# Optimization experiments

Measured on AMD Instinct MI355X. Metric: run time of the kernel, lower is better.

The kernel has to match this reference:

```python
import jax, jax.numpy as jnp
import numpy as np

N_NODES = 50000
N_REL = 3
N_EDGES = 800000
D_FEAT = 128
D_HID = 128  # == dim_embs so residual + concat dims line up
D_QUERY = 64


def setup_inputs() -> dict:
    key = jax.random.key(0)
    ks = jax.random.split(key, 8)
    s = 1.0 / np.sqrt(D_HID)
    return {
        "x": jax.random.normal(ks[0], (N_NODES, D_FEAT), dtype=jnp.float32),
        "edges": jax.random.randint(ks[1], (N_REL, 2, N_EDGES), 0, N_NODES, dtype=jnp.int64),
        "feat_w": jax.random.normal(ks[2], (D_FEAT, D_HID), dtype=jnp.float32) * s,
        "conv_w": jax.random.normal(ks[3], (2, N_REL, D_HID, D_HID), dtype=jnp.float32) * s,
        "conv_b": jax.random.normal(ks[4], (2, N_REL, D_HID), dtype=jnp.float32) * 0.01,
        "attn_w": jax.random.normal(ks[5], (2, D_HID, D_QUERY), dtype=jnp.float32) * s,
        "attn_q": jax.random.normal(ks[6], (2, D_QUERY), dtype=jnp.float32) * s,
        "concat_w": jax.random.normal(ks[7], (D_HID, 3 * D_HID), dtype=jnp.float32) * s,
    }


def reference(x, edges, feat_w, conv_w, conv_b, attn_w, attn_q, concat_w):
    N = x.shape[0]
    R = edges.shape[0]
    ones_e = jnp.ones((edges.shape[2],), dtype=x.dtype)

    def gconv(h, src, dst, W, b):
        # GraphConv with symmetric ('both') normalization + residual
        deg_out = jnp.clip(jax.ops.segment_sum(ones_e, src, num_segments=N), 1.0)
        deg_in = jnp.clip(jax.ops.segment_sum(ones_e, dst, num_segments=N), 1.0)
        m = (h * jax.lax.rsqrt(deg_out)[:, None]) @ W          # [N, D]
        agg = jax.ops.segment_sum(m[src], dst, num_segments=N)  # gather-scatter [E, D] -> [N, D]
        return agg * jax.lax.rsqrt(deg_in)[:, None] + b + h

    def het_layer(h, l):
        # per-relation conv, then attention-weighted aggregation across relations
        vals = jnp.stack([gconv(h, edges[r, 0], edges[r, 1], conv_w[l, r], conv_b[l, r])
                          for r in range(R)])                   # [R, N, D]
        keys = jnp.tanh(jnp.einsum('rnd,dq->rnq', vals, attn_w[l]))
        scores = jnp.einsum('rnq,q->rn', keys, attn_q[l])       # [R, N]
        attn = jax.nn.softmax(scores, axis=0)                   # softmax over relations
        return jnp.einsum('rn,rnd->nd', attn, vals), attn

    h0 = jnp.tanh(x @ feat_w)            # feature_trans + tanh
    h1, _ = het_layer(h0, 1)             # 1-hop path (convs[1] only)
    t, _ = het_layer(h0, 0)              # 2-hop path: convs[0]
    h2, attn = het_layer(t, 1)           # then convs[1]
    y = jnp.concatenate([h0, h1, h2], axis=-1) @ concat_w.T  # concat_weight (no bias)
    return y, attn.T                      # attn_res: [N, R]
```

## Files before the change

### kernel.cpp

```cpp
#include <hip/hip_runtime.h>

#define NN 50000
#define NE 800000
#define DD 128
#define DQ 64
#define NB 42
#define SL 19048
#define NW 25000

typedef __attribute__((ext_vector_type(8))) short short8_t;
typedef __attribute__((ext_vector_type(4))) float f32x4;

__device__ __forceinline__ int clampi(int v, int lo, int hi) {
  return v < lo ? lo : (v > hi ? hi : v);
}
__device__ __forceinline__ unsigned short f2bf(float f) {
  unsigned int u = __float_as_uint(f);
  return (unsigned short)((u + 0x7FFFu + ((u >> 16) & 1u)) >> 16);
}
__device__ __forceinline__ float bfl(unsigned int u) { return __uint_as_float(u << 16); }
__device__ __forceinline__ float bfh(unsigned int u) { return __uint_as_float(u & 0xFFFF0000u); }
__device__ __forceinline__ float b2f(short s) {
  return __uint_as_float(((unsigned int)(unsigned short)s) << 16);
}

__global__ __launch_bounds__(512) void hist6_kernel(
    const int* __restrict__ e, unsigned int* __restrict__ hist,
    unsigned short* __restrict__ rank) {
  __shared__ unsigned int lds[NW];
  const int b = blockIdx.x;
  const int c = blockIdx.y;
  const int r = c >> 1;
  const int a = c & 1;
  const int tid = threadIdx.x;
  for (int i = tid; i < NW; i += 512) lds[i] = 0u;
  __syncthreads();
  const size_t abase = (size_t)r * 2 * NE + (a ? 0 : NE);
  const int beg = b * SL, end = min(beg + SL, NE);
  if (a == 0) {
    unsigned short* rk = rank + (size_t)r * NE;
    for (int i = beg + tid; i < end; i += 512) {
      int v = clampi(e[abase + i], 0, NN - 1);
      unsigned int sh = (v & 1) * 16;
      unsigned int old = atomicAdd(&lds[v >> 1], 1u << sh);
      rk[i] = (unsigned short)((old >> sh) & 0xFFFFu);
    }
  } else {
    for (int i = beg + tid; i < end; i += 512) {
      int v = clampi(e[abase + i], 0, NN - 1);
      atomicAdd(&lds[v >> 1], 1u << ((v & 1) * 16));
    }
  }
  __syncthreads();
  unsigned int* outp = hist + ((size_t)c * NB + b) * NW;
  for (int i = tid; i < NW; i += 512) outp[i] = lds[i];
}

__global__ __launch_bounds__(256) void sumscan_kernel(
    const unsigned int* __restrict__ hist, int* __restrict__ rowptr,
    int* __restrict__ btot, float* __restrict__ rsqi, float* __restrict__ rsqo) {
  __shared__ int part[256];
  const int g = blockIdx.x;
  const int c = blockIdx.y;
  const int r = c >> 1, a = c & 1;
  const int t = threadIdx.x;
  int cntv[8];
  int s = 0;
  const int w0 = g * 1000 + t * 4;
  if (t < 250) {
#pragma unroll
    for (int j = 0; j < 4; ++j) {
      const unsigned int* hp = hist + (size_t)c * NB * NW + w0 + j;
      unsigned int lo = 0, hi = 0;
#pragma unroll 7
      for (int b = 0; b < NB; ++b) {
        unsigned int v = hp[(size_t)b * NW];
        lo += v & 0xFFFFu;
        hi += v >> 16;
      }
      cntv[2 * j] = (int)lo;
      cntv[2 * j + 1] = (int)hi;
      int n0 = 2 * (w0 + j), n1 = n0 + 1;
      float f0 = rsqrtf(fmaxf((float)lo, 1.0f));
      float f1 = rsqrtf(fmaxf((float)hi, 1.0f));
      if (a == 0) {
        rsqi[r * NN + n0] = f0;
        rsqi[r * NN + n1] = f1;
      } else {
        rsqo[r * NN + n0] = f0;
        rsqo[r * NN + n1] = f1;
      }
      s += (int)(lo + hi);
    }
  }
  if (a == 1) return;
  part[t] = s;
  __syncthreads();
  for (int off = 1; off < 256; off <<= 1) {
    int x = (t >= off) ? part[t - off] : 0;
    __syncthreads();
    part[t] += x;
    __syncthreads();
  }
  if (t < 250) {
    int excl = part[t] - s;
    int base = g * 2000 + t * 8;
#pragma unroll
    for (int j = 0; j < 8; ++j) {
      rowptr[r * (NN + 1) + base + j] = excl;
      excl += cntv[j];
    }
  }
  if (t == 255) btot[r * 25 + g] = part[255];
}

__global__ __launch_bounds__(64) void scanp2_kernel(
    const int* __restrict__ btot, int* __restrict__ boff, int* __restrict__ rowptr) {
  if (threadIdx.x == 0) {
    for (int r = 0; r < 3; ++r) {
      int run = 0;
      for (int b = 0; b < 25; ++b) {
        boff[r * 25 + b] = run;
        run += btot[r * 25 + b];
      }
      rowptr[r * (NN + 1) + NN] = run;
    }
  }
}

__global__ __launch_bounds__(256) void bases_kernel(
    const unsigned int* __restrict__ hist, const int* __restrict__ boff,
    int* __restrict__ rowptr, int* __restrict__ bases) {
  const int r = blockIdx.y;
  const int off = boff[r * 25 + blockIdx.x];
  for (int wl = threadIdx.x; wl < 1000; wl += 256) {
    int w = blockIdx.x * 1000 + wl;
    int n0 = 2 * w, n1 = n0 + 1;
    int run0 = rowptr[r * (NN + 1) + n0] + off;
    int run1 = rowptr[r * (NN + 1) + n1] + off;
    rowptr[r * (NN + 1) + n0] = run0;
    rowptr[r * (NN + 1) + n1] = run1;
    const unsigned int* hp = hist + (size_t)(r * 2) * NB * NW + w;
    int* bp = bases + (size_t)r * NB * NN;
#pragma unroll 7
    for (int b = 0; b < NB; ++b) {
      unsigned int v = hp[(size_t)b * NW];
      bp[(size_t)b * NN + n0] = run0;
      bp[(size_t)b * NN + n1] = run1;
      run0 += (int)(v & 0xFFFFu);
      run1 += (int)(v >> 16);
    }
  }
}

__global__ __launch_bounds__(256) void fillr_kernel(
    const int* __restrict__ e, const unsigned short* __restrict__ rank,
    const int* __restrict__ bases, int* __restrict__ col) {
  const int r = blockIdx.y;
  const int i = blockIdx.x * 256 + threadIdx.x;
  const size_t sbase = (size_t)r * 2 * NE;
  int s = clampi(e[sbase + i], 0, NN - 1);
  int d = clampi(e[sbase + NE + i], 0, NN - 1);
  int b = i / SL;
  int pos = clampi(bases[((size_t)r * NB + b) * NN + d] + (int)rank[(size_t)r * NE + i],
                   0, NE - 1);
  col[(size_t)r * NE + pos] = s;
}

__global__ __launch_bounds__(256) void prepw_kernel(
    const float* __restrict__ conv_w, const float* __restrict__ feat_w,
    const float* __restrict__ concat_w, const float* __restrict__ attn_w,
    unsigned short* __restrict__ fw) {
  const int i = blockIdx.x;
  if (i < 10) {
    unsigned short* dst = fw + (size_t)i * 16384;
    for (int e = threadIdx.x; e < 2048; e += 256) {
      int nt = e >> 8, ks = (e >> 6) & 3, lane = e & 63;
      int n = (lane & 15) + nt * 16;
      int kb = (lane >> 4) * 8 + ks * 32;
      unsigned int w[4];
#pragma unroll
      for (int jj = 0; jj < 4; ++jj) {
        int k0 = kb + 2 * jj, k1 = k0 + 1;
        float f0, f1;
        if (i < 6) {
          f0 = conv_w[(size_t)i * 16384 + (size_t)k0 * DD + n];
          f1 = conv_w[(size_t)i * 16384 + (size_t)k1 * DD + n];
        } else if (i == 6) {
          f0 = feat_w[(size_t)k0 * DD + n];
          f1 = feat_w[(size_t)k1 * DD + n];
        } else {
          int p = i - 7;
          f0 = concat_w[(size_t)n * 384 + p * DD + k0];
          f1 = concat_w[(size_t)n * 384 + p * DD + k1];
        }
        w[jj] = (unsigned int)f2bf(f0) | ((unsigned int)f2bf(f1) << 16);
      }
      ((uint4*)dst)[e] = make_uint4(w[0], w[1], w[2], w[3]);
    }
  } else {
    const int l = i - 10;
    unsigned short* dst = fw + (size_t)10 * 16384 + (size_t)l * 8192;
    for (int e = threadIdx.x; e < 1024; e += 256) {
      int nt = e >> 8, ks = (e >> 6) & 3, lane = e & 63;
      int n = (lane & 15) + nt * 16;
      int kb = (lane >> 4) * 8 + ks * 32;
      unsigned int w[4];
#pragma unroll
      for (int jj = 0; jj < 4; ++jj) {
        int k0 = kb + 2 * jj, k1 = k0 + 1;
        float f0 = attn_w[((size_t)l * DD + k0) * DQ + n];
        float f1 = attn_w[((size_t)l * DD + k1) * DQ + n];
        w[jj] = (unsigned int)f2bf(f0) | ((unsigned int)f2bf(f1) << 16);
      }
      ((uint4*)dst)[e] = make_uint4(w[0], w[1], w[2], w[3]);
    }
  }
}

template <int AFP32, int TANH, int EPI, int SIX>
__global__ __launch_bounds__(256) void mgemm_kernel(
    const void* __restrict__ Ap, const unsigned short* __restrict__ fw,
    const float* __restrict__ rsqi, const float* __restrict__ bias,
    const unsigned short* __restrict__ residb, unsigned short* __restrict__ Cb) {
  const size_t ND = (size_t)NN * DD;
  const int rel = blockIdx.y;
  const int wsel = SIX ? (rel + 3) % 6 : rel;
  const int arel = SIX ? rel % 3 : rel;
  const unsigned short* fwp = fw + (size_t)wsel * 16384;
  const float* rsqip = EPI ? rsqi + (size_t)arel * NN : nullptr;
  const float* biasp = EPI ? bias + (size_t)wsel * DD : nullptr;
  unsigned short* Cbp = Cb + (size_t)rel * ND;
  __shared__ unsigned short sF[16384];
  const int tid = threadIdx.x;
  {
    const float4* s = (const float4*)fwp;
    float4* d = (float4*)sF;
#pragma unroll
    for (int i = 0; i < 8; ++i) d[tid + i * 256] = s[tid + i * 256];
  }
  __syncthreads();
  const int w = tid >> 6, l = tid & 63, la = l & 15, gr = l >> 4;
  const int row0 = blockIdx.x * 128 + w * 32;
  if (row0 >= NN) return;
  const bool m1ok = (row0 + 32) <= NN;
  short8_t a[2][4];
#pragma unroll
  for (int m = 0; m < 2; ++m) {
    const int r = row0 + m * 16 + la;
    const bool ok = (m == 0) || m1ok;
    if (AFP32) {
      const float* ap = (const float*)Ap + (size_t)r * DD + gr * 8;
#pragma unroll
      for (int ks = 0; ks < 4; ++ks) {
        short8_t v = (short8_t)0;
        if (ok) {
          float4 x0 = *(const float4*)(ap + ks * 32);
          float4 x1 = *(const float4*)(ap + ks * 32 + 4);
          v[0] = (short)f2bf(x0.x); v[1] = (short)f2bf(x0.y);
          v[2] = (short)f2bf(x0.z); v[3] = (short)f2bf(x0.w);
          v[4] = (short)f2bf(x1.x); v[5] = (short)f2bf(x1.y);
          v[6] = (short)f2bf(x1.z); v[7] = (short)f2bf(x1.w);
        }
        a[m][ks] = v;
      }
    } else {
      const unsigned short* ap =
          (const unsigned short*)Ap + (size_t)arel * ND + (size_t)r * DD + gr * 8;
#pragma unroll
      for (int ks = 0; ks < 4; ++ks)
        a[m][ks] = ok ? *(const short8_t*)(ap + ks * 32) : (short8_t)0;
    }
  }
  f32x4 zero = {0.f, 0.f, 0.f, 0.f};
  f32x4 acc[2][8];
#pragma unroll
  for (int m = 0; m < 2; ++m)
#pragma unroll
    for (int nt = 0; nt < 8; ++nt) acc[m][nt] = zero;
#pragma unroll
  for (int nt = 0; nt < 8; ++nt) {
#pragma unroll
    for (int ks = 0; ks < 4; ++ks) {
      short8_t b = *(const short8_t*)(sF + ((nt * 4 + ks) * 64 + l) * 8);
      acc[0][nt] = __builtin_amdgcn_mfma_f32_16x16x32_bf16(a[0][ks], b, acc[0][nt], 0, 0, 0);
      acc[1][nt] = __builtin_amdgcn_mfma_f32_16x16x32_bf16(a[1][ks], b, acc[1][nt], 0, 0, 0);
    }
  }
#pragma unroll
  for (int m = 0; m < 2; ++m) {
    if (m == 1 && !m1ok) break;
#pragma unroll
    for (int rr = 0; rr < 4; ++rr) {
      const int row = row0 + m * 16 + gr * 4 + rr;
      const float sc = EPI ? rsqip[row] : 0.0f;
#pragma unroll
      for (int nt = 0; nt < 8; ++nt) {
        const int c0 = nt * 16 + la;
        float v = acc[m][nt][rr];
        if (TANH) v = tanhf(v);
        if (EPI) {
          float rv = __uint_as_float((unsigned int)residb[(size_t)row * DD + c0] << 16);
          v = fmaf(v, sc, biasp[c0] + rv);
        }
        Cbp[(size_t)row * DD + c0] = f2bf(v);
      }
    }
  }
}

__global__ __launch_bounds__(512) void mconcat_kernel(
    const unsigned short* __restrict__ h0b, const unsigned short* __restrict__ h1b,
    const unsigned short* __restrict__ h2b, const unsigned short* __restrict__ fwc,
    float* __restrict__ Y) {
  __shared__ unsigned short sF[3 * 16384];
  const int tid = threadIdx.x;
  {
    const float4* s = (const float4*)fwc;
    float4* d = (float4*)sF;
#pragma unroll
    for (int i = 0; i < 12; ++i) d[tid + i * 512] = s[tid + i * 512];
  }
  __syncthreads();
  const int w = tid >> 6, l = tid & 63, la = l & 15, gr = l >> 4;
  const int row0 = blockIdx.x * 256 + w * 32;
  if (row0 >= NN) return;
  const bool m1ok = (row0 + 32) <= NN;
  const unsigned short* hb[3] = {h0b, h1b, h2b};
  f32x4 zero = {0.f, 0.f, 0.f, 0.f};
  f32x4 acc[2][8];
#pragma unroll
  for (int m = 0; m < 2; ++m)
#pragma unroll
    for (int nt = 0; nt < 8; ++nt) acc[m][nt] = zero;
#pragma unroll
  for (int p = 0; p < 3; ++p) {
    short8_t a[2][4];
#pragma unroll
    for (int m = 0; m < 2; ++m) {
      const int r = row0 + m * 16 + la;
      const bool ok = (m == 0) || m1ok;
      const unsigned short* ap = hb[p] + (size_t)r * DD + gr * 8;
#pragma unroll
      for (int ks = 0; ks < 4; ++ks)
        a[m][ks] = ok ? *(const short8_t*)(ap + ks * 32) : (short8_t)0;
    }
    const unsigned short* sfp = sF + p * 16384;
#pragma unroll
    for (int nt = 0; nt < 8; ++nt) {
#pragma unroll
      for (int ks = 0; ks < 4; ++ks) {
        short8_t b = *(const short8_t*)(sfp + ((nt * 4 + ks) * 64 + l) * 8);
        acc[0][nt] = __builtin_amdgcn_mfma_f32_16x16x32_bf16(a[0][ks], b, acc[0][nt], 0, 0, 0);
        acc[1][nt] = __builtin_amdgcn_mfma_f32_16x16x32_bf16(a[1][ks], b, acc[1][nt], 0, 0, 0);
      }
    }
  }
#pragma unroll
  for (int m = 0; m < 2; ++m) {
    if (m == 1 && !m1ok) break;
#pragma unroll
    for (int rr = 0; rr < 4; ++rr) {
      const int row = row0 + m * 16 + gr * 4 + rr;
#pragma unroll
      for (int nt = 0; nt < 8; ++nt)
        Y[(size_t)row * DD + nt * 16 + la] = acc[m][nt][rr];
    }
  }
}

#define ACC8(A, V, C) \
  A[0] = fmaf(bfl((V).x), (C), A[0]); A[1] = fmaf(bfh((V).x), (C), A[1]); \
  A[2] = fmaf(bfl((V).y), (C), A[2]); A[3] = fmaf(bfh((V).y), (C), A[3]); \
  A[4] = fmaf(bfl((V).z), (C), A[4]); A[5] = fmaf(bfh((V).z), (C), A[5]); \
  A[6] = fmaf(bfl((V).w), (C), A[6]); A[7] = fmaf(bfh((V).w), (C), A[7]);

__global__ __launch_bounds__(256) void gatherb_kernel(
    const unsigned short* __restrict__ hb, const int* __restrict__ rowptr,
    const int* __restrict__ col, const float* __restrict__ rsqo,
    unsigned short* __restrict__ ub) {
  const size_t ND = (size_t)NN * DD;
  const int rel = blockIdx.y;
  rowptr += (size_t)rel * (NN + 1);
  col += (size_t)rel * NE;
  rsqo += (size_t)rel * NN;
  ub += (size_t)rel * ND;
  int gid = blockIdx.x * 256 + threadIdx.x;
  int n = gid >> 4;
  int lane = gid & 15;
  int e0 = clampi(rowptr[n], 0, NE);
  int e1 = clampi(rowptr[n + 1], e0, NE);
  const uint4* h4 = (const uint4*)hb;
  float a[8] = {0, 0, 0, 0, 0, 0, 0, 0}, b[8] = {0, 0, 0, 0, 0, 0, 0, 0};
  float c[8] = {0, 0, 0, 0, 0, 0, 0, 0}, d[8] = {0, 0, 0, 0, 0, 0, 0, 0};
  int e = e0;
  for (; e + 7 < e1; e += 8) {
    int s0 = clampi(col[e], 0, NN - 1), s1 = clampi(col[e + 1], 0, NN - 1);
    int s2 = clampi(col[e + 2], 0, NN - 1), s3 = clampi(col[e + 3], 0, NN - 1);
    int s4 = clampi(col[e + 4], 0, NN - 1), s5 = clampi(col[e + 5], 0, NN - 1);
    int s6 = clampi(col[e + 6], 0, NN - 1), s7 = clampi(col[e + 7], 0, NN - 1);
    float c0 = rsqo[s0], c1 = rsqo[s1], c2 = rsqo[s2], c3 = rsqo[s3];
    float c4 = rsqo[s4], c5 = rsqo[s5], c6 = rsqo[s6], c7 = rsqo[s7];
    uint4 v0 = h4[(size_t)s0 * 16 + lane];
    uint4 v1 = h4[(size_t)s1 * 16 + lane];
    uint4 v2 = h4[(size_t)s2 * 16 + lane];
    uint4 v3 = h4[(size_t)s3 * 16 + lane];
    uint4 v4 = h4[(size_t)s4 * 16 + lane];
    uint4 v5 = h4[(size_t)s5 * 16 + lane];
    uint4 v6 = h4[(size_t)s6 * 16 + lane];
    uint4 v7 = h4[(size_t)s7 * 16 + lane];
    ACC8(a, v0, c0) ACC8(b, v1, c1) ACC8(c, v2, c2) ACC8(d, v3, c3)
    ACC8(a, v4, c4) ACC8(b, v5, c5) ACC8(c, v6, c6) ACC8(d, v7, c7)
  }
  for (; e + 3 < e1; e += 4) {
    int s0 = clampi(col[e], 0, NN - 1), s1 = clampi(col[e + 1], 0, NN - 1);
    int s2 = clampi(col[e + 2], 0, NN - 1), s3 = clampi(col[e + 3], 0, NN - 1);
    float c0 = rsqo[s0], c1 = rsqo[s1], c2 = rsqo[s2], c3 = rsqo[s3];
    uint4 v0 = h4[(size_t)s0 * 16 + lane];
    uint4 v1 = h4[(size_t)s1 * 16 + lane];
    uint4 v2 = h4[(size_t)s2 * 16 + lane];
    uint4 v3 = h4[(size_t)s3 * 16 + lane];
    ACC8(a, v0, c0) ACC8(b, v1, c1) ACC8(c, v2, c2) ACC8(d, v3, c3)
  }
  for (; e < e1; ++e) {
    int s0 = clampi(col[e], 0, NN - 1);
    float c0 = rsqo[s0];
    uint4 v0 = h4[(size_t)s0 * 16 + lane];
    ACC8(a, v0, c0)
  }
#pragma unroll
  for (int j = 0; j < 8; ++j) a[j] += b[j] + c[j] + d[j];
  uint4 o;
  o.x = (unsigned int)f2bf(a[0]) | ((unsigned int)f2bf(a[1]) << 16);
  o.y = (unsigned int)f2bf(a[2]) | ((unsigned int)f2bf(a[3]) << 16);
  o.z = (unsigned int)f2bf(a[4]) | ((unsigned int)f2bf(a[5]) << 16);
  o.w = (unsigned int)f2bf(a[6]) | ((unsigned int)f2bf(a[7]) << 16);
  ((uint4*)ub)[gid] = o;
}

template <int TWO>
__global__ __launch_bounds__(256) void mscomb_kernel(
    const unsigned short* __restrict__ Vb, const unsigned short* __restrict__ faB,
    const float* __restrict__ AQB, unsigned short* __restrict__ houtB,
    float* __restrict__ attn_out) {
  const size_t ND = (size_t)NN * DD;
  const int y = TWO ? blockIdx.y : 0;
  const unsigned short* Vp = Vb + (TWO ? (size_t)y * 3 * ND : 0);
  const unsigned short* fa = TWO ? faB + (size_t)(1 - y) * 8192 : faB;
  const float* AQ = TWO ? AQB + (size_t)(1 - y) * DQ : AQB;
  unsigned short* houtb = TWO ? houtB + (size_t)y * ND : houtB;
  __shared__ unsigned short sF[8192];
  __shared__ float sS[4][3][32];
  const int tid = threadIdx.x;
  {
    const float4* s = (const float4*)fa;
    float4* d = (float4*)sF;
#pragma unroll
    for (int i = 0; i < 4; ++i) d[tid + i * 256] = s[tid + i * 256];
  }
  const int w = tid >> 6, l = tid & 63, la = l & 15, gr = l >> 4;
  int row0 = blockIdx.x * 128 + w * 32;
  if (row0 + 32 > NN) row0 = NN - 32;
  short8_t a[3][2][4];
#pragma unroll
  for (int r3 = 0; r3 < 3; ++r3) {
#pragma unroll
    for (int m = 0; m < 2; ++m) {
      const unsigned short* rp =
          Vp + (size_t)r3 * ND + (size_t)(row0 + m * 16 + la) * DD + gr * 8;
#pragma unroll
      for (int ks = 0; ks < 4; ++ks)
        a[r3][m][ks] = *(const short8_t*)(rp + ks * 32);
    }
  }
  __syncthreads();
  float q[4];
#pragma unroll
  for (int nt = 0; nt < 4; ++nt) q[nt] = AQ[la + nt * 16];
#pragma unroll
  for (int r3 = 0; r3 < 3; ++r3) {
    f32x4 zero = {0.f, 0.f, 0.f, 0.f};
    f32x4 acc[2][4];
#pragma unroll
    for (int m = 0; m < 2; ++m)
#pragma unroll
      for (int nt = 0; nt < 4; ++nt) acc[m][nt] = zero;
#pragma unroll
    for (int nt = 0; nt < 4; ++nt) {
#pragma unroll
      for (int ks = 0; ks < 4; ++ks) {
        short8_t b = *(const short8_t*)(sF + ((nt * 4 + ks) * 64 + l) * 8);
        acc[0][nt] = __builtin_amdgcn_mfma_f32_16x16x32_bf16(a[r3][0][ks], b, acc[0][nt], 0, 0, 0);
        acc[1][nt] = __builtin_amdgcn_mfma_f32_16x16x32_bf16(a[r3][1][ks], b, acc[1][nt], 0, 0, 0);
      }
    }
#pragma unroll
    for (int m = 0; m < 2; ++m) {
#pragma unroll
      for (int rr = 0; rr < 4; ++rr) {
        float p = tanhf(acc[m][0][rr]) * q[0] + tanhf(acc[m][1][rr]) * q[1] +
                  tanhf(acc[m][2][rr]) * q[2] + tanhf(acc[m][3][rr]) * q[3];
#pragma unroll
        for (int off = 1; off < 16; off <<= 1) p += __shfl_xor(p, off, 16);
        if (la == 0) sS[w][r3][m * 16 + gr * 4 + rr] = p;
      }
    }
  }
  __syncthreads();
#pragma unroll
  for (int m = 0; m < 2; ++m) {
    const int row = row0 + m * 16 + la;
    float s0 = sS[w][0][m * 16 + la];
    float s1 = sS[w][1][m * 16 + la];
    float s2 = sS[w][2][m * 16 + la];
    float mx = fmaxf(s0, fmaxf(s1, s2));
    float e0 = __expf(s0 - mx), e1 = __expf(s1 - mx), e2 = __expf(s2 - mx);
    float inv = 1.0f / (e0 + e1 + e2);
    float a0 = e0 * inv, a1 = e1 * inv, a2 = e2 * inv;
#pragma unroll
    for (int ks = 0; ks < 4; ++ks) {
      unsigned int ow[4];
#pragma unroll
      for (int jj = 0; jj < 4; ++jj) {
        float v0 = a0 * b2f(a[0][m][ks][2 * jj]) + a1 * b2f(a[1][m][ks][2 * jj]) +
                   a2 * b2f(a[2][m][ks][2 * jj]);
        float v1 = a0 * b2f(a[0][m][ks][2 * jj + 1]) + a1 * b2f(a[1][m][ks][2 * jj + 1]) +
                   a2 * b2f(a[2][m][ks][2 * jj + 1]);
        ow[jj] = (unsigned int)f2bf(v0) | ((unsigned int)f2bf(v1) << 16);
      }
      *(uint4*)(houtb + (size_t)row * DD + gr * 8 + ks * 32) =
          make_uint4(ow[0], ow[1], ow[2], ow[3]);
    }
    if (attn_out != nullptr) {
      attn_out[(size_t)row * 3 + 0] = a0;
      attn_out[(size_t)row * 3 + 1] = a1;
      attn_out[(size_t)row * 3 + 2] = a2;
    }
  }
}

extern "C" void kernel_launch(void* const* d_in, const int* in_sizes, int n_in,
                              void* d_out, int out_size, void* d_ws, size_t ws_size,
                              hipStream_t stream) {
  const float* x        = (const float*)d_in[0];
  const int*   edges    = (const int*)d_in[1];
  const float* feat_w   = (const float*)d_in[2];
  const float* conv_w   = (const float*)d_in[3];
  const float* conv_b   = (const float*)d_in[4];
  const float* attn_w   = (const float*)d_in[5];
  const float* attn_q   = (const float*)d_in[6];
  const float* concat_w = (const float*)d_in[7];
  float* out = (float*)d_out;

  float* ws = (float*)d_ws;
  float* rsqo = ws;
  float* rsqi = rsqo + 3 * NN;
  int* btot = (int*)(rsqi + 3 * NN);
  int* boff = btot + 80;
  int* cnt = boff + 96;
  int* rowptr = cnt + 3 * NN;
  int* col = rowptr + 3 * (NN + 1) + 13;
  const size_t ND = (size_t)NN * DD;
  float* P1 = (float*)(col + 3 * (size_t)NE);
  float* PA = P1 + ND;
  float* PB = PA + ND;
  unsigned short* U0 = (unsigned short*)(PB + ND);
  unsigned short* B0 = U0 + 3 * ND;
  unsigned short* B1 = B0 + ND;
  unsigned short* B2 = B1 + ND;
  unsigned short* fw = (unsigned short*)cnt;
  unsigned int* hist = (unsigned int*)PA;
  int* bases = (int*)PB;
  unsigned short* rank = (unsigned short*)P1;
  unsigned short* VbAll = (unsigned short*)P1;
  unsigned short* fa0 = fw + (size_t)10 * 16384;
  unsigned short* fa1 = fa0 + 8192;

  hist6_kernel<<<dim3(NB, 6), 512, 0, stream>>>(edges, hist, rank);
  sumscan_kernel<<<dim3(25, 6), 256, 0, stream>>>(hist, rowptr, btot, rsqi, rsqo);
  scanp2_kernel<<<1, 64, 0, stream>>>(btot, boff, rowptr);
  prepw_kernel<<<12, 256, 0, stream>>>(conv_w, feat_w, concat_w, attn_w, fw);
  bases_kernel<<<dim3(25, 3), 256, 0, stream>>>(hist, boff, rowptr, bases);
  fillr_kernel<<<dim3(3125, 3), 256, 0, stream>>>(edges, rank, bases, col);

  mgemm_kernel<1, 1, 0, 0><<<dim3(391, 1), 256, 0, stream>>>(
      x, fw + (size_t)6 * 16384, nullptr, nullptr, nullptr, B0);

  gatherb_kernel<<<dim3(3125, 3), 256, 0, stream>>>(B0, rowptr, col, rsqo, U0);

  mgemm_kernel<0, 0, 1, 1><<<dim3(391, 6), 256, 0, stream>>>(
      U0, fw, rsqi, conv_b, B0, VbAll);
  mscomb_kernel<1><<<dim3(391, 2), 256, 0, stream>>>(
      VbAll, fa0, attn_q, B1, nullptr);

  gatherb_kernel<<<dim3(3125, 3), 256, 0, stream>>>(B2, rowptr, col, rsqo, U0);
  mgemm_kernel<0, 0, 1, 0><<<dim3(391, 3), 256, 0, stream>>>(
      U0, fw + (size_t)3 * 16384, rsqi, conv_b + (size_t)3 * DD, B2, VbAll);
  mscomb_kernel<0><<<dim3(391, 1), 256, 0, stream>>>(
      VbAll, fa1, attn_q + DQ, U0, out + ND);

  mconcat_kernel<<<196, 512, 0, stream>>>(B0, B1, U0, fw + (size_t)7 * 16384, out);
}
```

Measured before the change: 453.0 us.

## Pack CSR histogram into 8-bit counters and fuse final combine with concat GEMM

The CSR build now uses 8-bit per-node counters packed four to a word, with twice as many edge slices. Ranks are stored as bytes and per-slice bases as byte deltas added to rowptr, which shrinks the histogram, rank and bases traffic. The last relation-attention combine is fused with the concat projection, so h2 is kept in registers and never written to or re-read from global memory. The risk is overflow if any node gets more than 255 edges in one slice, which is unlikely for random edges, and the fused kernel needs more LDS and registers.

```diff
diff --git a/kernel.cpp b/kernel.cpp
--- a/kernel.cpp
+++ b/kernel.cpp
@@ -4,9 +4,9 @@
 #define NE 800000
 #define DD 128
 #define DQ 64
-#define NB 42
-#define SL 19048
-#define NW 25000
+#define NB 84
+#define SL 9524
+#define NWW 12500
 
 typedef __attribute__((ext_vector_type(8))) short short8_t;
 typedef __attribute__((ext_vector_type(4))) float f32x4;
@@ -26,34 +26,34 @@
 
 __global__ __launch_bounds__(512) void hist6_kernel(
     const int* __restrict__ e, unsigned int* __restrict__ hist,
-    unsigned short* __restrict__ rank) {
-  __shared__ unsigned int lds[NW];
+    unsigned char* __restrict__ rank) {
+  __shared__ unsigned int lds[NWW];
   const int b = blockIdx.x;
   const int c = blockIdx.y;
   const int r = c >> 1;
   const int a = c & 1;
   const int tid = threadIdx.x;
-  for (int i = tid; i < NW; i += 512) lds[i] = 0u;
+  for (int i = tid; i < NWW; i += 512) lds[i] = 0u;
   __syncthreads();
   const size_t abase = (size_t)r * 2 * NE + (a ? 0 : NE);
   const int beg = b * SL, end = min(beg + SL, NE);
   if (a == 0) {
-    unsigned short* rk = rank + (size_t)r * NE;
+    unsigned char* rk = rank + (size_t)r * NE;
     for (int i = beg + tid; i < end; i += 512) {
       int v = clampi(e[abase + i], 0, NN - 1);
-      unsigned int sh = (v & 1) * 16;
-      unsigned int old = atomicAdd(&lds[v >> 1], 1u << sh);
-      rk[i] = (unsigned short)((old >> sh) & 0xFFFFu);
+      unsigned int sh = (v & 3) * 8;
+      unsigned int old = atomicAdd(&lds[v >> 2], 1u << sh);
+      rk[i] = (unsigned char)((old >> sh) & 0xFFu);
     }
   } else {
     for (int i = beg + tid; i < end; i += 512) {
       int v = clampi(e[abase + i], 0, NN - 1);
-      atomicAdd(&lds[v >> 1], 1u << ((v & 1) * 16));
-    }
-  }
-  __syncthreads();
-  unsigned int* outp = hist + ((size_t)c * NB + b) * NW;
-  for (int i = tid; i < NW; i += 512) outp[i] = lds[i];
+      atomicAdd(&lds[v >> 2], 1u << ((v & 3) * 8));
+    }
+  }
+  __syncthreads();
+  unsigned int* outp = hist + ((size_t)c * NB + b) * NWW;
+  for (int i = tid; i < NWW; i += 512) outp[i] = lds[i];
 }
 
 __global__ __launch_bounds__(256) void sumscan_kernel(
@@ -66,31 +66,29 @@
   const int t = threadIdx.x;
   int cntv[8];
   int s = 0;
-  const int w0 = g * 1000 + t * 4;
+  const int w0 = g * 500 + t * 2;
   if (t < 250) {
 #pragma unroll
-    for (int j = 0; j < 4; ++j) {
-      const unsigned int* hp = hist + (size_t)c * NB * NW + w0 + j;
-      unsigned int lo = 0, hi = 0;
-#pragma unroll 7
+    for (int j = 0; j < 2; ++j) {
+      const unsigned int* hp = hist + (size_t)c * NB * NWW + w0 + j;
+      unsigned int accA = 0, accB = 0;
+#pragma unroll 12
       for (int b = 0; b < NB; ++b) {
-        unsigned int v = hp[(size_t)b * NW];
-        lo += v & 0xFFFFu;
-        hi += v >> 16;
-      }
-      cntv[2 * j] = (int)lo;
-      cntv[2 * j + 1] = (int)hi;
-      int n0 = 2 * (w0 + j), n1 = n0 + 1;
-      float f0 = rsqrtf(fmaxf((float)lo, 1.0f));
-      float f1 = rsqrtf(fmaxf((float)hi, 1.0f));
-      if (a == 0) {
-        rsqi[r * NN + n0] = f0;
-        rsqi[r * NN + n1] = f1;
-      } else {
-        rsqo[r * NN + n0] = f0;
-        rsqo[r * NN + n1] = f1;
-      }
-      s += (int)(lo + hi);
+        unsigned int v = hp[(size_t)b * NWW];
+        accA += v & 0x00FF00FFu;
+        accB += (v >> 8) & 0x00FF00FFu;
+      }
+      int c0 = (int)(accA & 0xFFFFu), c2 = (int)(accA >> 16);
+      int c1 = (int)(accB & 0xFFFFu), c3 = (int)(accB >> 16);
+      cntv[4 * j + 0] = c0; cntv[4 * j + 1] = c1;
+      cntv[4 * j + 2] = c2; cntv[4 * j + 3] = c3;
+      int n0 = 4 * (w0 + j);
+      float* rq = (a == 0) ? rsqi : rsqo;
+      rq[r * NN + n0 + 0] = rsqrtf(fmaxf((float)c0, 1.0f));
+      rq[r * NN + n0 + 1] = rsqrtf(fmaxf((float)c1, 1.0f));
+      rq[r * NN + n0 + 2] = rsqrtf(fmaxf((float)c2, 1.0f));
+      rq[r * NN + n0 + 3] = rsqrtf(fmaxf((float)c3, 1.0f));
+      s += c0 + c1 + c2 + c3;
     }
   }
   if (a == 1) return;
@@ -130,40 +128,39 @@
 
 __global__ __launch_bounds__(256) void bases_kernel(
     const unsigned int* __restrict__ hist, const int* __restrict__ boff,
-    int* __restrict__ rowptr, int* __restrict__ bases) {
+    int* __restrict__ rowptr, unsigned int* __restrict__ delta32) {
   const int r = blockIdx.y;
-  const int off = boff[r * 25 + blockIdx.x];
-  for (int wl = threadIdx.x; wl < 1000; wl += 256) {
-    int w = blockIdx.x * 1000 + wl;
-    int n0 = 2 * w, n1 = n0 + 1;
-    int run0 = rowptr[r * (NN + 1) + n0] + off;
-    int run1 = rowptr[r * (NN + 1) + n1] + off;
-    rowptr[r * (NN + 1) + n0] = run0;
-    rowptr[r * (NN + 1) + n1] = run1;
-    const unsigned int* hp = hist + (size_t)(r * 2) * NB * NW + w;
-    int* bp = bases + (size_t)r * NB * NN;
-#pragma unroll 7
+  const int g = blockIdx.x;
+  const int off = boff[r * 25 + g];
+  for (int wl = threadIdx.x; wl < 500; wl += 256) {
+    int wi = g * 500 + wl;
+    int n0 = 4 * wi;
+#pragma unroll
+    for (int k = 0; k < 4; ++k) rowptr[r * (NN + 1) + n0 + k] += off;
+    const unsigned int* hp = hist + (size_t)(r * 2) * NB * NWW + wi;
+    unsigned int run = 0;
+#pragma unroll 12
     for (int b = 0; b < NB; ++b) {
-      unsigned int v = hp[(size_t)b * NW];
-      bp[(size_t)b * NN + n0] = run0;
-      bp[(size_t)b * NN + n1] = run1;
-      run0 += (int)(v & 0xFFFFu);
-      run1 += (int)(v >> 16);
+      delta32[((size_t)r * NB + b) * NWW + wi] = run;
+      run += hp[(size_t)b * NWW];
     }
   }
 }
 
 __global__ __launch_bounds__(256) void fillr_kernel(
-    const int* __restrict__ e, const unsigned short* __restrict__ rank,
-    const int* __restrict__ bases, int* __restrict__ col) {
+    const int* __restrict__ e, const unsigned char* __restrict__ rank,
+    const unsigned char* __restrict__ delta8, const int* __restrict__ rowptr,
+    int* __restrict__ col) {
   const int r = blockIdx.y;
   const int i = blockIdx.x * 256 + threadIdx.x;
   const size_t sbase = (size_t)r * 2 * NE;
   int s = clampi(e[sbase + i], 0, NN - 1);
   int d = clampi(e[sbase + NE + i], 0, NN - 1);
   int b = i / SL;
-  int pos = clampi(bases[((size_t)r * NB + b) * NN + d] + (int)rank[(size_t)r * NE + i],
-                   0, NE - 1);
+  int pos = rowptr[r * (NN + 1) + d] +
+            (int)delta8[((size_t)r * NB + b) * NN + d] +
+            (int)rank[(size_t)r * NE + i];
+  pos = clampi(pos, 0, NE - 1);
   col[(size_t)r * NE + pos] = s;
 }
 
@@ -305,66 +302,6 @@
         }
         Cbp[(size_t)row * DD + c0] = f2bf(v);
       }
-    }
-  }
-}
-
-__global__ __launch_bounds__(512) void mconcat_kernel(
-    const unsigned short* __restrict__ h0b, const unsigned short* __restrict__ h1b,
-    const unsigned short* __restrict__ h2b, const unsigned short* __restrict__ fwc,
-    float* __restrict__ Y) {
-  __shared__ unsigned short sF[3 * 16384];
-  const int tid = threadIdx.x;
-  {
-    const float4* s = (const float4*)fwc;
-    float4* d = (float4*)sF;
-#pragma unroll
-    for (int i = 0; i < 12; ++i) d[tid + i * 512] = s[tid + i * 512];
-  }
-  __syncthreads();
-  const int w = tid >> 6, l = tid & 63, la = l & 15, gr = l >> 4;
-  const int row0 = blockIdx.x * 256 + w * 32;
-  if (row0 >= NN) return;
-  const bool m1ok = (row0 + 32) <= NN;
-  const unsigned short* hb[3] = {h0b, h1b, h2b};
-  f32x4 zero = {0.f, 0.f, 0.f, 0.f};
-  f32x4 acc[2][8];
-#pragma unroll
-  for (int m = 0; m < 2; ++m)
-#pragma unroll
-    for (int nt = 0; nt < 8; ++nt) acc[m][nt] = zero;
-#pragma unroll
-  for (int p = 0; p < 3; ++p) {
-    short8_t a[2][4];
-#pragma unroll
-    for (int m = 0; m < 2; ++m) {
-      const int r = row0 + m * 16 + la;
-      const bool ok = (m == 0) || m1ok;
-      const unsigned short* ap = hb[p] + (size_t)r * DD + gr * 8;
-#pragma unroll
-      for (int ks = 0; ks < 4; ++ks)
-        a[m][ks] = ok ? *(const short8_t*)(ap + ks * 32) : (short8_t)0;
-    }
-    const unsigned short* sfp = sF + p * 16384;
-#pragma unroll
-    for (int nt = 0; nt < 8; ++nt) {
-#pragma unroll
-      for (int ks = 0; ks < 4; ++ks) {
-        short8_t b = *(const short8_t*)(sfp + ((nt * 4 + ks) * 64 + l) * 8);
-        acc[0][nt] = __builtin_amdgcn_mfma_f32_16x16x32_bf16(a[0][ks], b, acc[0][nt], 0, 0, 0);
-        acc[1][nt] = __builtin_amdgcn_mfma_f32_16x16x32_bf16(a[1][ks], b, acc[1][nt], 0, 0, 0);
-      }
-    }
-  }
-#pragma unroll
-  for (int m = 0; m < 2; ++m) {
-    if (m == 1 && !m1ok) break;
-#pragma unroll
-    for (int rr = 0; rr < 4; ++rr) {
-      const int row = row0 + m * 16 + gr * 4 + rr;
-#pragma unroll
-      for (int nt = 0; nt < 8; ++nt)
-        Y[(size_t)row * DD + nt * 16 + la] = acc[m][nt][rr];
     }
   }
 }
@@ -438,17 +375,15 @@
   ((uint4*)ub)[gid] = o;
 }
 
-template <int TWO>
 __global__ __launch_bounds__(256) void mscomb_kernel(
     const unsigned short* __restrict__ Vb, const unsigned short* __restrict__ faB,
-    const float* __restrict__ AQB, unsigned short* __restrict__ houtB,
-    float* __restrict__ attn_out) {
+    const float* __restrict__ AQB, unsigned short* __restrict__ houtB) {
   const size_t ND = (size_t)NN * DD;
-  const int y = TWO ? blockIdx.y : 0;
-  const unsigned short* Vp = Vb + (TWO ? (size_t)y * 3 * ND : 0);
-  const unsigned short* fa = TWO ? faB + (size_t)(1 - y) * 8192 : faB;
-  const float* AQ = TWO ? AQB + (size_t)(1 - y) * DQ : AQB;
-  unsigned short* houtb = TWO ? houtB + (size_t)y * ND : houtB;
+  const int y = blockIdx.y;
+  const unsigned short* Vp = Vb + (size_t)y * 3 * ND;
+  const unsigned short* fa = faB + (size_t)(1 - y) * 8192;
+  const float* AQ = AQB + (size_t)(1 - y) * DQ;
+  unsigned short* houtb = houtB + (size_t)y * ND;
   __shared__ unsigned short sF[8192];
   __shared__ float sS[4][3][32];
   const int tid = threadIdx.x;
@@ -531,10 +466,146 @@
       *(uint4*)(houtb + (size_t)row * DD + gr * 8 + ks * 32) =
           make_uint4(ow[0], ow[1], ow[2], ow[3]);
     }
-    if (attn_out != nullptr) {
-      attn_out[(size_t)row * 3 + 0] = a0;
-      attn_out[(size_t)row * 3 + 1] = a1;
-      attn_out[(size_t)row * 3 + 2] = a2;
+  }
+}
+
+__global__ __launch_bounds__(256) void mscombc_kernel(
+    const unsigned short* __restrict__ Vb, const unsigned short* __restrict__ fa,
+    const float* __restrict__ AQ, const unsigned short* __restrict__ h0b,
+    const unsigned short* __restrict__ h1b, const unsigned short* __restrict__ fwc,
+    float* __restrict__ Y, float* __restrict__ attn_out) {
+  const size_t ND = (size_t)NN * DD;
+  __shared__ unsigned short sF[8192];
+  __shared__ unsigned short sC[16384];
+  __shared__ float sS[4][3][32];
+  const int tid = threadIdx.x;
+  {
+    const float4* s = (const float4*)fa;
+    float4* d = (float4*)sF;
+#pragma unroll
+    for (int i = 0; i < 4; ++i) d[tid + i * 256] = s[tid + i * 256];
+  }
+  const int w = tid >> 6, l = tid & 63, la = l & 15, gr = l >> 4;
+  int row0 = blockIdx.x * 128 + w * 32;
+  if (row0 + 32 > NN) row0 = NN - 32;
+  short8_t a[3][2][4];
+#pragma unroll
+  for (int r3 = 0; r3 < 3; ++r3) {
+#pragma unroll
+    for (int m = 0; m < 2; ++m) {
+      const unsigned short* rp =
+          Vb + (size_t)r3 * ND + (size_t)(row0 + m * 16 + la) * DD + gr * 8;
+#pragma unroll
+      for (int ks = 0; ks < 4; ++ks)
+        a[r3][m][ks] = *(const short8_t*)(rp + ks * 32);
+    }
+  }
+  __syncthreads();
+  float q[4];
+#pragma unroll
+  for (int nt = 0; nt < 4; ++nt) q[nt] = AQ[la + nt * 16];
+#pragma unroll
+  for (int r3 = 0; r3 < 3; ++r3) {
+    f32x4 zero = {0.f, 0.f, 0.f, 0.f};
+    f32x4 acc[2][4];
+#pragma unroll
+    for (int m = 0; m < 2; ++m)
+#pragma unroll
+      for (int nt = 0; nt < 4; ++nt) acc[m][nt] = zero;
+#pragma unroll
+    for (int nt = 0; nt < 4; ++nt) {
+#pragma unroll
+      for (int ks = 0; ks < 4; ++ks) {
+        short8_t b = *(const short8_t*)(sF + ((nt * 4 + ks) * 64 + l) * 8);
+        acc[0][nt] = __builtin_amdgcn_mfma_f32_16x16x32_bf16(a[r3][0][ks], b, acc[0][nt], 0, 0, 0);
+        acc[1][nt] = __builtin_amdgcn_mfma_f32_16x16x32_bf16(a[r3][1][ks], b, acc[1][nt], 0, 0, 0);
+      }
+    }
+#pragma unroll
+    for (int m = 0; m < 2; ++m) {
+#pragma unroll
+      for (int rr = 0; rr < 4; ++rr) {
+        float p = tanhf(acc[m][0][rr]) * q[0] + tanhf(acc[m][1][rr]) * q[1] +
+                  tanhf(acc[m][2][rr]) * q[2] + tanhf(acc[m][3][rr]) * q[3];
+#pragma unroll
+        for (int off = 1; off < 16; off <<= 1) p += __shfl_xor(p, off, 16);
+        if (la == 0) sS[w][r3][m * 16 + gr * 4 + rr] = p;
+      }
+    }
+  }
+  __syncthreads();
+#pragma unroll
+  for (int m = 0; m < 2; ++m) {
+    const int row = row0 + m * 16 + la;
+    float s0 = sS[w][0][m * 16 + la];
+    float s1 = sS[w][1][m * 16 + la];
+    float s2 = sS[w][2][m * 16 + la];
+    float mx = fmaxf(s0, fmaxf(s1, s2));
+    float e0 = __expf(s0 - mx), e1 = __expf(s1 - mx), e2 = __expf(s2 - mx);
+    float inv = 1.0f / (e0 + e1 + e2);
+    float a0 = e0 * inv, a1 = e1 * inv, a2 = e2 * inv;
+#pragma unroll
+    for (int ks = 0; ks < 4; ++ks) {
+#pragma unroll
+      for (int jj = 0; jj < 8; ++jj) {
+        float v = a0 * b2f(a[0][m][ks][jj]) + a1 * b2f(a[1][m][ks][jj]) +
+                  a2 * b2f(a[2][m][ks][jj]);
+        a[0][m][ks][jj] = (short)f2bf(v);
+      }
+    }
+    attn_out[(size_t)row * 3 + 0] = a0;
+    attn_out[(size_t)row * 3 + 1] = a1;
+    attn_out[(size_t)row * 3 + 2] = a2;
+  }
+  f32x4 zero = {0.f, 0.f, 0.f, 0.f};
+  f32x4 yacc[2][8];
+#pragma unroll
+  for (int m = 0; m < 2; ++m)
+#pragma unroll
+    for (int nt = 0; nt < 8; ++nt) yacc[m][nt] = zero;
+#pragma unroll
+  for (int p = 0; p < 3; ++p) {
+    __syncthreads();
+    {
+      const float4* s = (const float4*)(fwc + (size_t)p * 16384);
+      float4* d = (float4*)sC;
+#pragma unroll
+      for (int i = 0; i < 8; ++i) d[tid + i * 256] = s[tid + i * 256];
+    }
+    __syncthreads();
+    short8_t af[2][4];
+    if (p == 2) {
+#pragma unroll
+      for (int m = 0; m < 2; ++m)
+#pragma unroll
+        for (int ks = 0; ks < 4; ++ks) af[m][ks] = a[0][m][ks];
+    } else {
+      const unsigned short* hp = (p == 0) ? h0b : h1b;
+#pragma unroll
+      for (int m = 0; m < 2; ++m) {
+        const unsigned short* rp = hp + (size_t)(row0 + m * 16 + la) * DD + gr * 8;
+#pragma unroll
+        for (int ks = 0; ks < 4; ++ks) af[m][ks] = *(const short8_t*)(rp + ks * 32);
+      }
+    }
+#pragma unroll
+    for (int nt = 0; nt < 8; ++nt) {
+#pragma unroll
+      for (int ks = 0; ks < 4; ++ks) {
+        short8_t b = *(const short8_t*)(sC + ((nt * 4 + ks) * 64 + l) * 8);
+        yacc[0][nt] = __builtin_amdgcn_mfma_f32_16x16x32_bf16(af[0][ks], b, yacc[0][nt], 0, 0, 0);
+        yacc[1][nt] = __builtin_amdgcn_mfma_f32_16x16x32_bf16(af[1][ks], b, yacc[1][nt], 0, 0, 0);
+      }
+    }
+  }
+#pragma unroll
+  for (int m = 0; m < 2; ++m) {
+#pragma unroll
+    for (int rr = 0; rr < 4; ++rr) {
+      const int row = row0 + m * 16 + gr * 4 + rr;
+#pragma unroll
+      for (int nt = 0; nt < 8; ++nt)
+        Y[(size_t)row * DD + nt * 16 + la] = yacc[m][nt][rr];
     }
   }
 }
@@ -570,18 +641,18 @@
   unsigned short* B2 = B1 + ND;
   unsigned short* fw = (unsigned short*)cnt;
   unsigned int* hist = (unsigned int*)PA;
-  int* bases = (int*)PB;
-  unsigned short* rank = (unsigned short*)P1;
+  unsigned char* delta8 = (unsigned char*)PB;
+  unsigned char* rank8 = (unsigned char*)P1;
   unsigned short* VbAll = (unsigned short*)P1;
   unsigned short* fa0 = fw + (size_t)10 * 16384;
   unsigned short* fa1 = fa0 + 8192;
 
-  hist6_kernel<<<dim3(NB, 6), 512, 0, stream>>>(edges, hist, rank);
+  hist6_kernel<<<dim3(NB, 6), 512, 0, stream>>>(edges, hist, rank8);
   sumscan_kernel<<<dim3(25, 6), 256, 0, stream>>>(hist, rowptr, btot, rsqi, rsqo);
   scanp2_kernel<<<1, 64, 0, stream>>>(btot, boff, rowptr);
   prepw_kernel<<<12, 256, 0, stream>>>(conv_w, feat_w, concat_w, attn_w, fw);
-  bases_kernel<<<dim3(25, 3), 256, 0, stream>>>(hist, boff, rowptr, bases);
-  fillr_kernel<<<dim3(3125, 3), 256, 0, stream>>>(edges, rank, bases, col);
+  bases_kernel<<<dim3(25, 3), 256, 0, stream>>>(hist, boff, rowptr, (unsigned int*)delta8);
+  fillr_kernel<<<dim3(3125, 3), 256, 0, stream>>>(edges, rank8, delta8, rowptr, col);
 
   mgemm_kernel<1, 1, 0, 0><<<dim3(391, 1), 256, 0, stream>>>(
       x, fw + (size_t)6 * 16384, nullptr, nullptr, nullptr, B0);
@@ -590,14 +661,11 @@
 
   mgemm_kernel<0, 0, 1, 1><<<dim3(391, 6), 256, 0, stream>>>(
       U0, fw, rsqi, conv_b, B0, VbAll);
-  mscomb_kernel<1><<<dim3(391, 2), 256, 0, stream>>>(
-      VbAll, fa0, attn_q, B1, nullptr);
+  mscomb_kernel<<<dim3(391, 2), 256, 0, stream>>>(VbAll, fa0, attn_q, B1);
 
   gatherb_kernel<<<dim3(3125, 3), 256, 0, stream>>>(B2, rowptr, col, rsqo, U0);
   mgemm_kernel<0, 0, 1, 0><<<dim3(391, 3), 256, 0, stream>>>(
       U0, fw + (size_t)3 * 16384, rsqi, conv_b + (size_t)3 * DD, B2, VbAll);
-  mscomb_kernel<0><<<dim3(391, 1), 256, 0, stream>>>(
-      VbAll, fa1, attn_q + DQ, U0, out + ND);
-
-  mconcat_kernel<<<196, 512, 0, stream>>>(B0, B1, U0, fw + (size_t)7 * 16384, out);
-}
+  mscombc_kernel<<<391, 256, 0, stream>>>(
+      VbAll, fa1, attn_q + DQ, B0, B1, fw + (size_t)7 * 16384, out, out + ND);
+}
```

New measurement: 463.7 us. 2.4% more time.
